# Kernel optimization log

Hardware: AMD Instinct MI355X
Metric: run time of the kernel (lower is better)

The kernel has to match this reference:

```python
import jax, jax.numpy as jnp
import numpy as np

B, SEQ, D = 4, 1024, 1024
H = 16
HD = D // H            # 64, matches cos/sin last dim
S_COLS, TOPK = 8, 2
INTER = 768            # find_multiple(round(1.0 * D * 2 / 3), 256)
EPS = 1e-5


def setup_inputs() -> dict:
    key = jax.random.key(0)
    ks = jax.random.split(key, 6)
    hidden_states = jax.random.normal(ks[0], (B, SEQ, D), jnp.float32)
    # RoPE tables (standard rotary, theta=10000)
    inv_freq = 1.0 / (10000.0 ** (jnp.arange(0, HD, 2, dtype=jnp.float32) / HD))
    freqs = jnp.outer(jnp.arange(SEQ, dtype=jnp.float32), inv_freq)
    emb = jnp.concatenate([freqs, freqs], axis=-1)  # [SEQ, HD]
    cos, sin = jnp.cos(emb), jnp.sin(emb)
    Wr = jax.random.normal(ks[1], (S_COLS, D), jnp.float32) * 0.02
    temperature = jnp.ones((1,), jnp.float32)
    # Stacked per-column TransformerBlock params (bias-free linears)
    Wqkv = jax.random.normal(ks[2], (S_COLS, D, 3 * D), jnp.float32) * 0.02
    Wo = jax.random.normal(ks[3], (S_COLS, D, D), jnp.float32) * 0.02
    Wgu = jax.random.normal(ks[4], (S_COLS, D, 2 * INTER), jnp.float32) * 0.02
    Wd = jax.random.normal(ks[5], (S_COLS, INTER, D), jnp.float32) * 0.02
    return dict(hidden_states=hidden_states, cos=cos, sin=sin, Wr=Wr,
                temperature=temperature, Wqkv=Wqkv, Wo=Wo, Wgu=Wgu, Wd=Wd)


def _rms_norm(x):
    return x * jax.lax.rsqrt(jnp.mean(x * x, axis=-1, keepdims=True) + EPS)


def _rotate_half(x):
    x1, x2 = jnp.split(x, 2, axis=-1)
    return jnp.concatenate([-x2, x1], axis=-1)


def _columns_forward(x, Wqkv, Wo, Wgu, Wd, cos, sin):
    # x: [n, seq, D] dispatched sequences; params gathered per dispatch entry [n, ...]
    n, seq, d = x.shape
    qkv = jnp.einsum('nsd,nde->nse', x, Wqkv)
    q, k, v = jnp.split(qkv, 3, axis=-1)
    q = q.reshape(n, seq, H, HD)
    k = k.reshape(n, seq, H, HD)
    v = v.reshape(n, seq, H, HD)
    c = cos[None, :, None, :]
    s = sin[None, :, None, :]
    q = q * c + _rotate_half(q) * s
    k = k * c + _rotate_half(k) * s
    scores = jnp.einsum('nqhd,nkhd->nhqk', q, k) / jnp.sqrt(jnp.asarray(HD, x.dtype))
    attn = jax.nn.softmax(scores, axis=-1)  # non-causal (HRM-style block)
    ctx = jnp.einsum('nhqk,nkhd->nqhd', attn, v).reshape(n, seq, d)
    attn_out = jnp.einsum('nsd,nde->nse', ctx, Wo)
    x = _rms_norm(x + attn_out)                      # post-norm residual
    gu = jnp.einsum('nsd,nde->nse', x, Wgu)
    gate, up = jnp.split(gu, 2, axis=-1)
    mlp_out = jnp.einsum('nsi,nid->nsd', jax.nn.silu(gate) * up, Wd)
    return _rms_norm(x + mlp_out)


def reference(hidden_states, cos, sin, Wr, temperature, Wqkv, Wo, Wgu, Wd):
    Bn = hidden_states.shape[0]
    temp = jnp.clip(temperature, 0.1, 10.0)
    routing_logits = (hidden_states.mean(axis=1) @ Wr.T) / temp   # [B, S]
    topk_vals, topk_idx = jax.lax.top_k(routing_logits, TOPK)
    weights = jax.nn.softmax(topk_vals, axis=-1)                  # [B, k]
    flat_idx = topk_idx.reshape(-1)                               # [B*k] expert ids
    flat_w = weights.reshape(-1)
    sample_idx = jnp.repeat(jnp.arange(Bn), TOPK)                 # [B*k]
    # Sparse dispatch: exactly B*k block forwards via per-entry param gather
    x_disp = hidden_states[sample_idx]
    col_out = _columns_forward(x_disp, Wqkv[flat_idx], Wo[flat_idx],
                               Wgu[flat_idx], Wd[flat_idx], cos, sin)
    result = jnp.zeros_like(hidden_states).at[sample_idx].add(
        flat_w[:, None, None] * col_out)
    return result, routing_logits
```

## Files before the change

kernel.cpp:

```cpp
#include <hip/hip_runtime.h>
#include <hip/hip_bf16.h>
#include <math.h>

#define B_     4
#define SEQ_   1024
#define D_     1024
#define H_     16
#define NE_    8
#define INTER_ 768
#define EPS_   1e-5f

typedef unsigned short u16;
typedef __attribute__((ext_vector_type(8))) short s8v;
typedef __attribute__((ext_vector_type(4))) short s4v;
typedef __attribute__((ext_vector_type(4))) float f4v;
typedef __attribute__((ext_vector_type(4))) unsigned short u16x4;
typedef __attribute__((ext_vector_type(8))) unsigned short u16x8;

__device__ __forceinline__ u16 f2bf(float x) {
    union { float f; unsigned u; } c; c.f = x;
    unsigned r = (c.u + 0x7FFFu + ((c.u >> 16) & 1u)) >> 16;
    return (u16)r;
}
__device__ __forceinline__ float bf2f(u16 h) {
    union { unsigned u; float f; } c; c.u = ((unsigned)h) << 16;
    return c.f;
}
__device__ __forceinline__ unsigned pk2(float a, float b) {
    union { float f; unsigned u; } x, y; x.f = a; y.f = b;
    return ((x.u + 0x8000u) >> 16) | ((y.u + 0x8000u) & 0xffff0000u);
}

#define GLDS16(gp, lp) \
    __builtin_amdgcn_global_load_lds((const __attribute__((address_space(1))) unsigned int*)(gp), \
                                     (__attribute__((address_space(3))) unsigned int*)(lp), 16, 0, 0)

__global__ void route1(const float* __restrict__ hidden, float* __restrict__ part) {
    int b = blockIdx.x, ch = blockIdx.y, t = threadIdx.x;
    const float* xb = hidden + (size_t)b * SEQ_ * D_ + (size_t)ch * 32 * D_;
    float4 acc = make_float4(0.f, 0.f, 0.f, 0.f);
    for (int r = 0; r < 32; ++r) {
        float4 v = *(const float4*)&xb[(size_t)r * D_ + t * 4];
        acc.x += v.x; acc.y += v.y; acc.z += v.z; acc.w += v.w;
    }
    *(float4*)&part[((size_t)(b * 32 + ch)) * D_ + t * 4] = acc;
}

__global__ void route2(const float* __restrict__ part, const float* __restrict__ Wr,
                       const float* __restrict__ temp, float* __restrict__ out_logits,
                       int* __restrict__ flat_idx, float* __restrict__ flat_w) {
    __shared__ float col[1024];
    __shared__ float sm[8];
    int b = blockIdx.x, t = threadIdx.x;
    float4 s = make_float4(0.f, 0.f, 0.f, 0.f);
    for (int ch = 0; ch < 32; ++ch) {
        float4 v = *(const float4*)&part[((size_t)(b * 32 + ch)) * D_ + t * 4];
        s.x += v.x; s.y += v.y; s.z += v.z; s.w += v.w;
    }
    col[t * 4 + 0] = s.x * (1.f / 1024.f);
    col[t * 4 + 1] = s.y * (1.f / 1024.f);
    col[t * 4 + 2] = s.z * (1.f / 1024.f);
    col[t * 4 + 3] = s.w * (1.f / 1024.f);
    __syncthreads();
    int j = t >> 5, d0 = t & 31;
    float p = 0.f;
    for (int d = d0; d < 1024; d += 32) p += col[d] * Wr[j * 1024 + d];
    for (int off = 16; off >= 1; off >>= 1) p += __shfl_down(p, off, 32);
    if (d0 == 0) sm[j] = p;
    __syncthreads();
    if (t == 0) {
        float tc = temp[0];
        tc = fminf(fmaxf(tc, 0.1f), 10.0f);
        float lg[8];
        for (int jj = 0; jj < 8; ++jj) {
            lg[jj] = sm[jj] / tc;
            out_logits[b * 8 + jj] = lg[jj];
        }
        int i0 = 0; float v0 = lg[0];
        for (int jj = 1; jj < 8; ++jj) if (lg[jj] > v0) { v0 = lg[jj]; i0 = jj; }
        int i1 = -1; float v1 = -1e30f;
        for (int jj = 0; jj < 8; ++jj) if (jj != i0 && lg[jj] > v1) { v1 = lg[jj]; i1 = jj; }
        float e1 = expf(v1 - v0);
        flat_idx[2 * b]     = i0;
        flat_idx[2 * b + 1] = i1;
        flat_w[2 * b]       = 1.0f / (1.0f + e1);
        flat_w[2 * b + 1]   = e1 / (1.0f + e1);
    }
}

__global__ __launch_bounds__(256) void wtrans(const float* __restrict__ W, u16* __restrict__ Wt,
                                              int K, int N) {
    __shared__ float tile[64][65];
    int e = blockIdx.z;
    int k0 = blockIdx.y * 64, n0 = blockIdx.x * 64;
    const float* Wp = W + (size_t)e * K * N;
    u16* Wtp = Wt + (size_t)e * K * N;
    int t = threadIdx.x;
    int kk = t >> 4, ns = t & 15;
#pragma unroll
    for (int p = 0; p < 4; ++p) {
        float4 v = *(const float4*)&Wp[(size_t)(k0 + kk + p * 16) * N + n0 + ns * 4];
        tile[kk + p * 16][ns * 4 + 0] = v.x;
        tile[kk + p * 16][ns * 4 + 1] = v.y;
        tile[kk + p * 16][ns * 4 + 2] = v.z;
        tile[kk + p * 16][ns * 4 + 3] = v.w;
    }
    __syncthreads();
    int nn = t >> 3, ks = t & 7;
#pragma unroll
    for (int p = 0; p < 2; ++p) {
        u16x8 o;
#pragma unroll
        for (int jj = 0; jj < 8; ++jj) o[jj] = f2bf(tile[ks * 8 + jj][nn + p * 32]);
        *(u16x8*)&Wtp[(size_t)(n0 + nn + p * 32) * K + k0 + ks * 8] = o;
    }
}

__global__ void cast_hidden(const float* __restrict__ x, u16* __restrict__ xb) {
    size_t i = (size_t)blockIdx.x * 256 + threadIdx.x;
    float4 v = *(const float4*)&x[i * 4];
    u16x4 o = {f2bf(v.x), f2bf(v.y), f2bf(v.z), f2bf(v.w)};
    *(u16x4*)&xb[i * 4] = o;
}

#define GEMM_CORE(A, Wt, K)                                                                 \
    f4v acc[4][4];                                                                          \
    _Pragma("unroll") for (int i = 0; i < 4; ++i)                                           \
        _Pragma("unroll") for (int jj = 0; jj < 4; ++jj) acc[i][jj] = (f4v){0.f,0.f,0.f,0.f}; \
    for (int k0 = 0; k0 < K; k0 += 32) {                                                    \
        _Pragma("unroll") for (int it = 0; it < 2; ++it) {                                  \
            int p = it * 256 + w * 64 + lane;                                               \
            int row = p >> 2, seg = (p & 3) ^ ((row >> 1) & 3);                             \
            GLDS16(A  + (size_t)(m0 + row) * K + k0 + seg * 8, As + (size_t)(it*256 + w*64) * 8); \
            GLDS16(Wt + (size_t)(n0 + row) * K + k0 + seg * 8, Bs + (size_t)(it*256 + w*64) * 8); \
        }                                                                                   \
        __syncthreads();                                                                    \
        s8v af[4], bfr[4];                                                                  \
        _Pragma("unroll") for (int ti = 0; ti < 4; ++ti) {                                  \
            int r = wm + ti * 16 + c;                                                       \
            af[ti]  = *(const s8v*)&As[r * 32 + (g ^ ((r >> 1) & 3)) * 8];                   \
        }                                                                                   \
        _Pragma("unroll") for (int tj = 0; tj < 4; ++tj) {                                  \
            int r = wn + tj * 16 + c;                                                       \
            bfr[tj] = *(const s8v*)&Bs[r * 32 + (g ^ ((r >> 1) & 3)) * 8];                   \
        }                                                                                   \
        _Pragma("unroll") for (int ti = 0; ti < 4; ++ti)                                    \
            _Pragma("unroll") for (int tj = 0; tj < 4; ++tj)                                \
                acc[ti][tj] = __builtin_amdgcn_mfma_f32_16x16x32_bf16(af[ti], bfr[tj], acc[ti][tj], 0, 0, 0); \
        __syncthreads();                                                                    \
    }

template<int OUTBF>
__global__ __launch_bounds__(256) void gemm_bf16(const u16* __restrict__ Abase,
                                                 const u16* __restrict__ Wtbase,
                                                 void* __restrict__ Cb,
                                                 const int* __restrict__ flat_idx,
                                                 int M, int N, int K, int aDiv) {
    __shared__ __align__(16) u16 As[128 * 32];
    __shared__ __align__(16) u16 Bs[128 * 32];
    int e = blockIdx.z;
    const u16* A  = Abase + (size_t)(e / aDiv) * M * K;
    const u16* Wt = Wtbase + (size_t)flat_idx[e] * N * K;
    int m0 = blockIdx.y * 128, n0 = blockIdx.x * 128;
    int t = threadIdx.x, lane = t & 63, w = t >> 6;
    int g = lane >> 4, c = lane & 15;
    int wm = (w >> 1) * 64, wn = (w & 1) * 64;

    GEMM_CORE(A, Wt, K)

    if (OUTBF) {
        u16* C = (u16*)Cb + (size_t)e * M * N;
#pragma unroll
        for (int ti = 0; ti < 4; ++ti)
#pragma unroll
            for (int tj = 0; tj < 4; ++tj)
#pragma unroll
                for (int i = 0; i < 4; ++i)
                    C[(size_t)(m0 + wm + ti * 16 + g * 4 + i) * N + n0 + wn + tj * 16 + c] = f2bf(acc[ti][tj][i]);
    } else {
        float* C = (float*)Cb + (size_t)e * M * N;
#pragma unroll
        for (int ti = 0; ti < 4; ++ti)
#pragma unroll
            for (int tj = 0; tj < 4; ++tj)
#pragma unroll
                for (int i = 0; i < 4; ++i)
                    C[(size_t)(m0 + wm + ti * 16 + g * 4 + i) * N + n0 + wn + tj * 16 + c] = acc[ti][tj][i];
    }
}

__global__ __launch_bounds__(256) void gemm_qkv(const u16* __restrict__ Abase,
                                                const u16* __restrict__ Wtbase,
                                                const int* __restrict__ flat_idx,
                                                const float* __restrict__ cosb,
                                                const float* __restrict__ sinb,
                                                u16* __restrict__ Qb, u16* __restrict__ Kb,
                                                u16* __restrict__ Vb) {
    __shared__ __align__(16) u16 As[128 * 32];
    __shared__ __align__(16) u16 Bs[128 * 32];
    const int K = 1024, N = 3072;
    int e = blockIdx.z;
    const u16* A  = Abase + (size_t)(e >> 1) * 1024 * K;
    const u16* Wt = Wtbase + (size_t)flat_idx[e] * N * K;
    int m0 = blockIdx.y * 128, n0 = blockIdx.x * 128;
    int t = threadIdx.x, lane = t & 63, w = t >> 6;
    int g = lane >> 4, c = lane & 15;
    int wm = (w >> 1) * 64, wn = (w & 1) * 64;

    GEMM_CORE(A, Wt, K)

    int col0 = n0 + wn;
    int sb = m0 + wm + g * 4;
    if (col0 < 2048) {
        bool isq = col0 < 1024;
        u16* dst = isq ? Qb : Kb;
        int h = (col0 & 1023) >> 6;
        const float scl = isq ? 0.125f * 1.44269504f : 1.0f;
#pragma unroll
        for (int ti = 0; ti < 4; ++ti)
#pragma unroll
            for (int i = 0; i < 4; ++i) {
                int s = sb + ti * 16 + i;
                size_t ob = ((size_t)(e * 1024) + s) * 1024 + h * 64;
#pragma unroll
                for (int tj = 0; tj < 2; ++tj) {
                    int d = tj * 16 + c;
                    float x1 = acc[ti][tj][i], x2 = acc[ti][tj + 2][i];
                    float c1 = cosb[s * 64 + d],      s1 = sinb[s * 64 + d];
                    float c2 = cosb[s * 64 + d + 32], s2 = sinb[s * 64 + d + 32];
                    dst[ob + d]      = f2bf((x1 * c1 - x2 * s1) * scl);
                    dst[ob + d + 32] = f2bf((x2 * c2 + x1 * s2) * scl);
                }
            }
    } else {
        int vcol = col0 - 2048;
#pragma unroll
        for (int ti = 0; ti < 4; ++ti)
#pragma unroll
            for (int tj = 0; tj < 4; ++tj)
#pragma unroll
                for (int i = 0; i < 4; ++i)
                    Vb[((size_t)(e * 1024) + sb + ti * 16 + i) * 1024 + vcol + tj * 16 + c] = f2bf(acc[ti][tj][i]);
    }
}

__global__ __launch_bounds__(256) void vtrans(const u16* __restrict__ Vb, u16* __restrict__ Vtg) {
    __shared__ __align__(16) u16 tile[64 * 72];
    int s0 = blockIdx.x * 64;
    int eh = blockIdx.y;
    int e = eh >> 4, h = eh & 15;
    int t = threadIdx.x;
#pragma unroll
    for (int it = 0; it < 2; ++it) {
        int p = it * 256 + t;
        int sr = p >> 3, ds = p & 7;
        u16x8 v = *(const u16x8*)&Vb[((size_t)(e * 1024) + s0 + sr) * 1024 + h * 64 + ds * 8];
        *(u16x8*)&tile[sr * 72 + ds * 8] = v;
    }
    __syncthreads();
#pragma unroll
    for (int it = 0; it < 2; ++it) {
        int p = it * 256 + t;
        int d = p >> 3, ks = p & 7;
        u16x8 o;
#pragma unroll
        for (int jj = 0; jj < 8; ++jj) o[jj] = tile[(ks * 8 + jj) * 72 + d];
        *(u16x8*)&Vtg[((size_t)((e * 16 + h) * 64) + d) * 1024 + s0 + ks * 8] = o;
    }
}

__global__ __launch_bounds__(256) void attn_mfma(const u16* __restrict__ Qb, const u16* __restrict__ Kb,
                                                 const u16* __restrict__ Vtg, u16* __restrict__ ctx) {
    __shared__ __align__(16) u16 Ks[64 * 64];
    __shared__ __align__(16) u16 Vt[64 * 64];
    int e = blockIdx.x, h = blockIdx.y, qt = blockIdx.z;
    int t = threadIdx.x, lane = t & 63, w = t >> 6;
    int g = lane >> 4, c = lane & 15;
    int q0 = qt * 64 + w * 16;

    s8v qf[2];
#pragma unroll
    for (int ks = 0; ks < 2; ++ks)
        qf[ks] = *(const s8v*)&Qb[((size_t)(e * 1024) + q0 + c) * 1024 + h * 64 + ks * 32 + g * 8];

    f4v O[4];
#pragma unroll
    for (int tj = 0; tj < 4; ++tj) O[tj] = (f4v){0.f, 0.f, 0.f, 0.f};
    f4v liacc = (f4v){0.f, 0.f, 0.f, 0.f};
    const s4v vone = {(short)0x3F80, (short)0x3F80, (short)0x3F80, (short)0x3F80};

    for (int kt = 0; kt < 16; ++kt) {
#pragma unroll
        for (int it = 0; it < 2; ++it) {
            int p = it * 256 + w * 64 + lane;
            int row = p >> 3, ss = p & 7;
            GLDS16(Kb + ((size_t)(e * 1024 + kt * 64 + row)) * 1024 + h * 64 + (ss ^ (row & 7)) * 8,
                   Ks + (size_t)(it * 256 + w * 64) * 8);
            GLDS16(Vtg + ((size_t)((e * 16 + h) * 64 + row)) * 1024 + kt * 64 + (ss ^ (row & 7)) * 8,
                   Vt + (size_t)(it * 256 + w * 64) * 8);
        }
        __syncthreads();

        f4v st[4];
#pragma unroll
        for (int tj = 0; tj < 4; ++tj) st[tj] = (f4v){0.f, 0.f, 0.f, 0.f};
#pragma unroll
        for (int ks = 0; ks < 2; ++ks)
#pragma unroll
            for (int tj = 0; tj < 4; ++tj) {
                int kvl = tj * 16 + c;
                s8v kf = *(const s8v*)&Ks[kvl * 64 + (((ks * 4 + g) ^ (kvl & 7)) * 8)];
                st[tj] = __builtin_amdgcn_mfma_f32_16x16x32_bf16(kf, qf[ks], st[tj], 0, 0, 0);
            }

        s4v pf[4];
#pragma unroll
        for (int tj = 0; tj < 4; ++tj) {
            float p0 = __builtin_amdgcn_exp2f(st[tj][0]);
            float p1 = __builtin_amdgcn_exp2f(st[tj][1]);
            float p2 = __builtin_amdgcn_exp2f(st[tj][2]);
            float p3 = __builtin_amdgcn_exp2f(st[tj][3]);
            union { unsigned u[2]; s4v v; } pu;
            pu.u[0] = pk2(p0, p1);
            pu.u[1] = pk2(p2, p3);
            pf[tj] = pu.v;
        }

#pragma unroll
        for (int tjC = 0; tjC < 4; ++tjC) {
            liacc = __builtin_amdgcn_mfma_f32_16x16x16bf16_1k(pf[tjC], vone, liacc, 0, 0, 0);
#pragma unroll
            for (int tjd = 0; tjd < 4; ++tjd) {
                int d = tjd * 16 + c;
                int sd = tjC * 2 + (g >> 1);
                s4v vf = *(const s4v*)&Vt[d * 64 + ((sd ^ (d & 7)) * 8) + (g & 1) * 4];
                O[tjd] = __builtin_amdgcn_mfma_f32_16x16x16bf16_1k(pf[tjC], vf, O[tjd], 0, 0, 0);
            }
        }
        __syncthreads();
    }
#pragma unroll
    for (int i = 0; i < 4; ++i) {
        float linv = 1.0f / liacc[i];
        size_t rbase = ((size_t)(e * 1024) + q0 + g * 4 + i) * 1024 + h * 64;
#pragma unroll
        for (int tjd = 0; tjd < 4; ++tjd)
            ctx[rbase + tjd * 16 + c] = f2bf(O[tjd][i] * linv);
    }
}

__global__ void add_rmsnorm(const float* __restrict__ hidden, const float* __restrict__ ao,
                            u16* __restrict__ xnb) {
    int row = blockIdx.x;
    int e = row >> 10;
    int b = e >> 1;
    int s = row & 1023;
    const float* xr = hidden + (((size_t)b * SEQ_ + s) << 10);
    const float* ar = ao + ((size_t)row << 10);
    u16* o = xnb + ((size_t)row << 10);
    int t = threadIdx.x;
    float v[4];
    float ss = 0.f;
#pragma unroll
    for (int i = 0; i < 4; ++i) {
        v[i] = xr[t + i * 256] + ar[t + i * 256];
        ss += v[i] * v[i];
    }
    for (int off = 32; off >= 1; off >>= 1) ss += __shfl_down(ss, off, 64);
    __shared__ float wred[4];
    if ((t & 63) == 0) wred[t >> 6] = ss;
    __syncthreads();
    float tot = wred[0] + wred[1] + wred[2] + wred[3];
    float scale = rsqrtf(tot * (1.0f / 1024.0f) + EPS_);
#pragma unroll
    for (int i = 0; i < 4; ++i) o[t + i * 256] = f2bf(v[i] * scale);
}

__global__ void silu_mul(const u16* __restrict__ gub, u16* __restrict__ act) {
    int idx = blockIdx.x * 256 + threadIdx.x;
    int col8 = idx % 96;
    int row  = idx / 96;
    u16x8 gv = *(const u16x8*)&gub[(size_t)row * 1536 + col8 * 8];
    u16x8 uv = *(const u16x8*)&gub[(size_t)row * 1536 + 768 + col8 * 8];
    u16x8 o;
#pragma unroll
    for (int jj = 0; jj < 8; ++jj) {
        float gt = bf2f(gv[jj]), u = bf2f(uv[jj]);
        o[jj] = f2bf(gt / (1.f + __expf(-gt)) * u);
    }
    *(u16x8*)&act[(size_t)row * 768 + col8 * 8] = o;
}

__global__ void final_kernel(const u16* __restrict__ xnb, const float* __restrict__ mlp,
                             const float* __restrict__ flat_w, float* __restrict__ out) {
    int row = blockIdx.x;
    int b = row >> 10;
    int s = row & 1023;
    int t = threadIdx.x;
    __shared__ float wred[4];
    float res[4] = {0.f, 0.f, 0.f, 0.f};
    for (int j = 0; j < 2; ++j) {
        int e = 2 * b + j;
        size_t off = (((size_t)e * SEQ_ + s) << 10);
        const u16* xr = xnb + off;
        const float* mr = mlp + off;
        float v[4];
        float ss = 0.f;
#pragma unroll
        for (int i = 0; i < 4; ++i) {
            v[i] = bf2f(xr[t + i * 256]) + mr[t + i * 256];
            ss += v[i] * v[i];
        }
        for (int off2 = 32; off2 >= 1; off2 >>= 1) ss += __shfl_down(ss, off2, 64);
        if ((t & 63) == 0) wred[t >> 6] = ss;
        __syncthreads();
        float tot = wred[0] + wred[1] + wred[2] + wred[3];
        float scale = rsqrtf(tot * (1.0f / 1024.0f) + EPS_);
        float wgt = flat_w[e];
#pragma unroll
        for (int i = 0; i < 4; ++i) res[i] += wgt * v[i] * scale;
        __syncthreads();
    }
    float* o = out + ((size_t)row << 10);
#pragma unroll
    for (int i = 0; i < 4; ++i) o[t + i * 256] = res[i];
}

extern "C" void kernel_launch(void* const* d_in, const int* in_sizes, int n_in,
                              void* d_out, int out_size, void* d_ws, size_t ws_size,
                              hipStream_t stream) {
    const float* hidden = (const float*)d_in[0];
    const float* cosb   = (const float*)d_in[1];
    const float* sinb   = (const float*)d_in[2];
    const float* Wr     = (const float*)d_in[3];
    const float* temp   = (const float*)d_in[4];
    const float* Wqkv   = (const float*)d_in[5];
    const float* Wo     = (const float*)d_in[6];
    const float* Wgu    = (const float*)d_in[7];
    const float* Wd     = (const float*)d_in[8];
    float* out = (float*)d_out;
    float* out_logits = out + (size_t)B_ * SEQ_ * D_;

    char* base = (char*)d_ws;
    int*   flat_idx = (int*)base;
    float* flat_w   = (float*)(base + 128);
    float* routeP   = (float*)(base + 4096);
    size_t off = (size_t)1 << 20;
    u16* WqkvT = (u16*)(base + off); off += (size_t)8 * 3072 * 1024 * 2;
    u16* WoT   = (u16*)(base + off); off += (size_t)8 * 1024 * 1024 * 2;
    u16* WguT  = (u16*)(base + off); off += (size_t)8 * 1536 * 1024 * 2;
    u16* WdT   = (u16*)(base + off); off += (size_t)8 * 1024 * 768 * 2;
    u16* hb    = (u16*)(base + off); off += (size_t)4 * 1024 * 1024 * 2;
    u16* scr   = (u16*)(base + off); off += (size_t)8 * 1024 * 3072 * 2;
    u16* Qb    = (u16*)(base + off); off += (size_t)8 * 1024 * 1024 * 2;
    u16* Kb    = (u16*)(base + off); off += (size_t)8 * 1024 * 1024 * 2;
    u16* Vtg   = (u16*)(base + off); off += (size_t)8 * 1024 * 1024 * 2;
    u16* ctxb  = (u16*)(base + off); off += (size_t)8 * 1024 * 1024 * 2;
    float* R1  = (float*)(base + off); off += (size_t)8 * 1024 * 1024 * 4;
    u16* xnb   = (u16*)(base + off); off += (size_t)8 * 1024 * 1024 * 2;
    u16* gub   = scr;
    u16* actb  = scr + (size_t)8 * 1024 * 1536;
    u16* Vb    = (u16*)R1;

    route1<<<dim3(4, 32), 256, 0, stream>>>(hidden, routeP);
    route2<<<4, 256, 0, stream>>>(routeP, Wr, temp, out_logits, flat_idx, flat_w);
    cast_hidden<<<4096, 256, 0, stream>>>(hidden, hb);
    wtrans<<<dim3(48, 16, 8), 256, 0, stream>>>(Wqkv, WqkvT, 1024, 3072);
    wtrans<<<dim3(16, 16, 8), 256, 0, stream>>>(Wo, WoT, 1024, 1024);
    wtrans<<<dim3(24, 16, 8), 256, 0, stream>>>(Wgu, WguT, 1024, 1536);
    wtrans<<<dim3(16, 12, 8), 256, 0, stream>>>(Wd, WdT, 768, 1024);

    gemm_qkv<<<dim3(24, 8, 8), 256, 0, stream>>>(hb, WqkvT, flat_idx, cosb, sinb, Qb, Kb, Vb);
    vtrans<<<dim3(16, 128), 256, 0, stream>>>(Vb, Vtg);
    attn_mfma<<<dim3(8, 16, 16), 256, 0, stream>>>(Qb, Kb, Vtg, ctxb);
    gemm_bf16<0><<<dim3(8, 8, 8), 256, 0, stream>>>(ctxb, WoT, R1, flat_idx, 1024, 1024, 1024, 1);
    add_rmsnorm<<<NE_ * SEQ_, 256, 0, stream>>>(hidden, R1, xnb);
    gemm_bf16<1><<<dim3(12, 8, 8), 256, 0, stream>>>(xnb, WguT, gub, flat_idx, 1024, 1536, 1024, 1);
    silu_mul<<<3072, 256, 0, stream>>>(gub, actb);
    gemm_bf16<0><<<dim3(8, 8, 8), 256, 0, stream>>>(actb, WdT, R1, flat_idx, 1024, 1024, 768, 1);
    final_kernel<<<B_ * SEQ_, 256, 0, stream>>>(xnb, R1, flat_w, out);
}
```

Measured before the change: 573.2 us.

## Fuse SiLU into gate/up GEMM, merge weight transposes, bf16 intermediates

Several unrelated changes. The hidden-state cast moves into the routing reduction kernel, and the four weight-transpose launches merge into one kernel. That kernel interleaves the gate/up columns in 16-wide groups so the gate/up GEMM epilogue can apply SiLU*up directly, which removes the separate silu_mul pass and its intermediate buffer. The GEMM outputs for the attention projection and down projection become bf16 instead of fp32, and the norm kernels use vectorized loads. This reduces memory traffic and launch count, at the cost of extra bf16 rounding on the residual paths.

```diff
diff --git a/kernel.cpp b/kernel.cpp
--- a/kernel.cpp
+++ b/kernel.cpp
@@ -35,13 +35,17 @@
     __builtin_amdgcn_global_load_lds((const __attribute__((address_space(1))) unsigned int*)(gp), \
                                      (__attribute__((address_space(3))) unsigned int*)(lp), 16, 0, 0)
 
-__global__ void route1(const float* __restrict__ hidden, float* __restrict__ part) {
+__global__ void route1(const float* __restrict__ hidden, float* __restrict__ part,
+                       u16* __restrict__ hb) {
     int b = blockIdx.x, ch = blockIdx.y, t = threadIdx.x;
     const float* xb = hidden + (size_t)b * SEQ_ * D_ + (size_t)ch * 32 * D_;
+    u16* ho = hb + (size_t)b * SEQ_ * D_ + (size_t)ch * 32 * D_;
     float4 acc = make_float4(0.f, 0.f, 0.f, 0.f);
     for (int r = 0; r < 32; ++r) {
         float4 v = *(const float4*)&xb[(size_t)r * D_ + t * 4];
         acc.x += v.x; acc.y += v.y; acc.z += v.z; acc.w += v.w;
+        u16x4 o = {f2bf(v.x), f2bf(v.y), f2bf(v.z), f2bf(v.w)};
+        *(u16x4*)&ho[(size_t)r * D_ + t * 4] = o;
     }
     *(float4*)&part[((size_t)(b * 32 + ch)) * D_ + t * 4] = acc;
 }
@@ -88,11 +92,25 @@
     }
 }
 
-__global__ __launch_bounds__(256) void wtrans(const float* __restrict__ W, u16* __restrict__ Wt,
-                                              int K, int N) {
+__global__ __launch_bounds__(256) void wtrans_all(const float* __restrict__ Wqkv,
+                                                  const float* __restrict__ Wo,
+                                                  const float* __restrict__ Wgu,
+                                                  const float* __restrict__ Wd,
+                                                  u16* __restrict__ WqkvT, u16* __restrict__ WoT,
+                                                  u16* __restrict__ WguT, u16* __restrict__ WdT) {
+    int bid = blockIdx.x;
+    const float* W; u16* Wt; int K, N, nx, gu = 0;
+    if (bid < 6144)      { W = Wqkv; Wt = WqkvT; K = 1024; N = 3072; nx = 48; }
+    else if (bid < 8192) { bid -= 6144;  W = Wo;  Wt = WoT;  K = 1024; N = 1024; nx = 16; }
+    else if (bid < 11264){ bid -= 8192;  W = Wgu; Wt = WguT; K = 1024; N = 1536; nx = 24; gu = 1; }
+    else                 { bid -= 11264; W = Wd;  Wt = WdT;  K = 768;  N = 1024; nx = 16; }
+    int x = bid % nx; bid /= nx;
+    int ny = K >> 6;
+    int y = bid % ny;
+    int e = bid / ny;
+
     __shared__ float tile[64][65];
-    int e = blockIdx.z;
-    int k0 = blockIdx.y * 64, n0 = blockIdx.x * 64;
+    int k0 = y * 64, n0 = x * 64;
     const float* Wp = W + (size_t)e * K * N;
     u16* Wtp = Wt + (size_t)e * K * N;
     int t = threadIdx.x;
@@ -109,18 +127,15 @@
     int nn = t >> 3, ks = t & 7;
 #pragma unroll
     for (int p = 0; p < 2; ++p) {
+        int n = n0 + nn + p * 32;
+        int nd = n;
+        if (gu) nd = (n < 768) ? ((n >> 4) << 5) + (n & 15)
+                               : (((n - 768) >> 4) << 5) + 16 + (n & 15);
         u16x8 o;
 #pragma unroll
         for (int jj = 0; jj < 8; ++jj) o[jj] = f2bf(tile[ks * 8 + jj][nn + p * 32]);
-        *(u16x8*)&Wtp[(size_t)(n0 + nn + p * 32) * K + k0 + ks * 8] = o;
-    }
-}
-
-__global__ void cast_hidden(const float* __restrict__ x, u16* __restrict__ xb) {
-    size_t i = (size_t)blockIdx.x * 256 + threadIdx.x;
-    float4 v = *(const float4*)&x[i * 4];
-    u16x4 o = {f2bf(v.x), f2bf(v.y), f2bf(v.z), f2bf(v.w)};
-    *(u16x4*)&xb[i * 4] = o;
+        *(u16x8*)&Wtp[(size_t)nd * K + k0 + ks * 8] = o;
+    }
 }
 
 #define GEMM_CORE(A, Wt, K)                                                                 \
@@ -150,10 +165,9 @@
         __syncthreads();                                                                    \
     }
 
-template<int OUTBF>
 __global__ __launch_bounds__(256) void gemm_bf16(const u16* __restrict__ Abase,
                                                  const u16* __restrict__ Wtbase,
-                                                 void* __restrict__ Cb,
+                                                 u16* __restrict__ Cb,
                                                  const int* __restrict__ flat_idx,
                                                  int M, int N, int K, int aDiv) {
     __shared__ __align__(16) u16 As[128 * 32];
@@ -168,25 +182,14 @@
 
     GEMM_CORE(A, Wt, K)
 
-    if (OUTBF) {
-        u16* C = (u16*)Cb + (size_t)e * M * N;
-#pragma unroll
-        for (int ti = 0; ti < 4; ++ti)
-#pragma unroll
-            for (int tj = 0; tj < 4; ++tj)
-#pragma unroll
-                for (int i = 0; i < 4; ++i)
-                    C[(size_t)(m0 + wm + ti * 16 + g * 4 + i) * N + n0 + wn + tj * 16 + c] = f2bf(acc[ti][tj][i]);
-    } else {
-        float* C = (float*)Cb + (size_t)e * M * N;
-#pragma unroll
-        for (int ti = 0; ti < 4; ++ti)
-#pragma unroll
-            for (int tj = 0; tj < 4; ++tj)
-#pragma unroll
-                for (int i = 0; i < 4; ++i)
-                    C[(size_t)(m0 + wm + ti * 16 + g * 4 + i) * N + n0 + wn + tj * 16 + c] = acc[ti][tj][i];
-    }
+    u16* C = Cb + (size_t)e * M * N;
+#pragma unroll
+    for (int ti = 0; ti < 4; ++ti)
+#pragma unroll
+        for (int tj = 0; tj < 4; ++tj)
+#pragma unroll
+            for (int i = 0; i < 4; ++i)
+                C[(size_t)(m0 + wm + ti * 16 + g * 4 + i) * N + n0 + wn + tj * 16 + c] = f2bf(acc[ti][tj][i]);
 }
 
 __global__ __launch_bounds__(256) void gemm_qkv(const u16* __restrict__ Abase,
@@ -244,6 +247,40 @@
     }
 }
 
+__global__ __launch_bounds__(256) void gemm_wgu_silu(const u16* __restrict__ Abase,
+                                                     const u16* __restrict__ Wtbase,
+                                                     u16* __restrict__ act,
+                                                     const int* __restrict__ flat_idx) {
+    __shared__ __align__(16) u16 As[128 * 32];
+    __shared__ __align__(16) u16 Bs[128 * 32];
+    const int K = 1024, N = 1536;
+    int e = blockIdx.z;
+    const u16* A  = Abase + (size_t)e * 1024 * K;
+    const u16* Wt = Wtbase + (size_t)flat_idx[e] * N * K;
+    int m0 = blockIdx.y * 128, n0 = blockIdx.x * 128;
+    int t = threadIdx.x, lane = t & 63, w = t >> 6;
+    int g = lane >> 4, c = lane & 15;
+    int wm = (w >> 1) * 64, wn = (w & 1) * 64;
+
+    GEMM_CORE(A, Wt, K)
+
+    int col0 = n0 + wn;
+    int oc0 = (col0 >> 1) + c;
+    int sb = m0 + wm + g * 4;
+#pragma unroll
+    for (int ti = 0; ti < 4; ++ti)
+#pragma unroll
+        for (int i = 0; i < 4; ++i) {
+            size_t rb = ((size_t)(e * 1024) + sb + ti * 16 + i) * 768;
+#pragma unroll
+            for (int pr = 0; pr < 2; ++pr) {
+                float gt = acc[ti][pr * 2][i];
+                float up = acc[ti][pr * 2 + 1][i];
+                act[rb + oc0 + pr * 16] = f2bf(gt / (1.f + __expf(-gt)) * up);
+            }
+        }
+}
+
 __global__ __launch_bounds__(256) void vtrans(const u16* __restrict__ Vb, u16* __restrict__ Vtg) {
     __shared__ __align__(16) u16 tile[64 * 72];
     int s0 = blockIdx.x * 64;
@@ -349,21 +386,23 @@
     }
 }
 
-__global__ void add_rmsnorm(const float* __restrict__ hidden, const float* __restrict__ ao,
+__global__ void add_rmsnorm(const u16* __restrict__ hb, const u16* __restrict__ aob,
                             u16* __restrict__ xnb) {
     int row = blockIdx.x;
     int e = row >> 10;
     int b = e >> 1;
     int s = row & 1023;
-    const float* xr = hidden + (((size_t)b * SEQ_ + s) << 10);
-    const float* ar = ao + ((size_t)row << 10);
+    const u16* xr = hb + (((size_t)b * SEQ_ + s) << 10);
+    const u16* ar = aob + ((size_t)row << 10);
     u16* o = xnb + ((size_t)row << 10);
     int t = threadIdx.x;
+    u16x4 xv = *(const u16x4*)&xr[t * 4];
+    u16x4 av = *(const u16x4*)&ar[t * 4];
     float v[4];
     float ss = 0.f;
 #pragma unroll
     for (int i = 0; i < 4; ++i) {
-        v[i] = xr[t + i * 256] + ar[t + i * 256];
+        v[i] = bf2f(xv[i]) + bf2f(av[i]);
         ss += v[i] * v[i];
     }
     for (int off = 32; off >= 1; off >>= 1) ss += __shfl_down(ss, off, 64);
@@ -372,26 +411,13 @@
     __syncthreads();
     float tot = wred[0] + wred[1] + wred[2] + wred[3];
     float scale = rsqrtf(tot * (1.0f / 1024.0f) + EPS_);
-#pragma unroll
-    for (int i = 0; i < 4; ++i) o[t + i * 256] = f2bf(v[i] * scale);
-}
-
-__global__ void silu_mul(const u16* __restrict__ gub, u16* __restrict__ act) {
-    int idx = blockIdx.x * 256 + threadIdx.x;
-    int col8 = idx % 96;
-    int row  = idx / 96;
-    u16x8 gv = *(const u16x8*)&gub[(size_t)row * 1536 + col8 * 8];
-    u16x8 uv = *(const u16x8*)&gub[(size_t)row * 1536 + 768 + col8 * 8];
-    u16x8 o;
-#pragma unroll
-    for (int jj = 0; jj < 8; ++jj) {
-        float gt = bf2f(gv[jj]), u = bf2f(uv[jj]);
-        o[jj] = f2bf(gt / (1.f + __expf(-gt)) * u);
-    }
-    *(u16x8*)&act[(size_t)row * 768 + col8 * 8] = o;
-}
-
-__global__ void final_kernel(const u16* __restrict__ xnb, const float* __restrict__ mlp,
+    u16x4 ov;
+#pragma unroll
+    for (int i = 0; i < 4; ++i) ov[i] = f2bf(v[i] * scale);
+    *(u16x4*)&o[t * 4] = ov;
+}
+
+__global__ void final_kernel(const u16* __restrict__ xnb, const u16* __restrict__ mlpb,
                              const float* __restrict__ flat_w, float* __restrict__ out) {
     int row = blockIdx.x;
     int b = row >> 10;
@@ -402,13 +428,13 @@
     for (int j = 0; j < 2; ++j) {
         int e = 2 * b + j;
         size_t off = (((size_t)e * SEQ_ + s) << 10);
-        const u16* xr = xnb + off;
-        const float* mr = mlp + off;
+        u16x4 xv = *(const u16x4*)&xnb[off + t * 4];
+        u16x4 mv = *(const u16x4*)&mlpb[off + t * 4];
         float v[4];
         float ss = 0.f;
 #pragma unroll
         for (int i = 0; i < 4; ++i) {
-            v[i] = bf2f(xr[t + i * 256]) + mr[t + i * 256];
+            v[i] = bf2f(xv[i]) + bf2f(mv[i]);
             ss += v[i] * v[i];
         }
         for (int off2 = 32; off2 >= 1; off2 >>= 1) ss += __shfl_down(ss, off2, 64);
@@ -422,8 +448,7 @@
         __syncthreads();
     }
     float* o = out + ((size_t)row << 10);
-#pragma unroll
-    for (int i = 0; i < 4; ++i) o[t + i * 256] = res[i];
+    *(float4*)&o[t * 4] = make_float4(res[0], res[1], res[2], res[3]);
 }
 
 extern "C" void kernel_launch(void* const* d_in, const int* in_sizes, int n_in,
@@ -451,32 +476,26 @@
     u16* WguT  = (u16*)(base + off); off += (size_t)8 * 1536 * 1024 * 2;
     u16* WdT   = (u16*)(base + off); off += (size_t)8 * 1024 * 768 * 2;
     u16* hb    = (u16*)(base + off); off += (size_t)4 * 1024 * 1024 * 2;
-    u16* scr   = (u16*)(base + off); off += (size_t)8 * 1024 * 3072 * 2;
     u16* Qb    = (u16*)(base + off); off += (size_t)8 * 1024 * 1024 * 2;
     u16* Kb    = (u16*)(base + off); off += (size_t)8 * 1024 * 1024 * 2;
+    u16* Vb    = (u16*)(base + off); off += (size_t)8 * 1024 * 1024 * 2;
     u16* Vtg   = (u16*)(base + off); off += (size_t)8 * 1024 * 1024 * 2;
     u16* ctxb  = (u16*)(base + off); off += (size_t)8 * 1024 * 1024 * 2;
-    float* R1  = (float*)(base + off); off += (size_t)8 * 1024 * 1024 * 4;
+    u16* aob   = (u16*)(base + off); off += (size_t)8 * 1024 * 1024 * 2;
     u16* xnb   = (u16*)(base + off); off += (size_t)8 * 1024 * 1024 * 2;
-    u16* gub   = scr;
-    u16* actb  = scr + (size_t)8 * 1024 * 1536;
-    u16* Vb    = (u16*)R1;
-
-    route1<<<dim3(4, 32), 256, 0, stream>>>(hidden, routeP);
+    u16* actb  = (u16*)(base + off); off += (size_t)8 * 1024 * 768 * 2;
+    u16* mlpb  = (u16*)(base + off); off += (size_t)8 * 1024 * 1024 * 2;
+
+    route1<<<dim3(4, 32), 256, 0, stream>>>(hidden, routeP, hb);
     route2<<<4, 256, 0, stream>>>(routeP, Wr, temp, out_logits, flat_idx, flat_w);
-    cast_hidden<<<4096, 256, 0, stream>>>(hidden, hb);
-    wtrans<<<dim3(48, 16, 8), 256, 0, stream>>>(Wqkv, WqkvT, 1024, 3072);
-    wtrans<<<dim3(16, 16, 8), 256, 0, stream>>>(Wo, WoT, 1024, 1024);
-    wtrans<<<dim3(24, 16, 8), 256, 0, stream>>>(Wgu, WguT, 1024, 1536);
-    wtrans<<<dim3(16, 12, 8), 256, 0, stream>>>(Wd, WdT, 768, 1024);
+    wtrans_all<<<12800, 256, 0, stream>>>(Wqkv, Wo, Wgu, Wd, WqkvT, WoT, WguT, WdT);
 
     gemm_qkv<<<dim3(24, 8, 8), 256, 0, stream>>>(hb, WqkvT, flat_idx, cosb, sinb, Qb, Kb, Vb);
     vtrans<<<dim3(16, 128), 256, 0, stream>>>(Vb, Vtg);
     attn_mfma<<<dim3(8, 16, 16), 256, 0, stream>>>(Qb, Kb, Vtg, ctxb);
-    gemm_bf16<0><<<dim3(8, 8, 8), 256, 0, stream>>>(ctxb, WoT, R1, flat_idx, 1024, 1024, 1024, 1);
-    add_rmsnorm<<<NE_ * SEQ_, 256, 0, stream>>>(hidden, R1, xnb);
-    gemm_bf16<1><<<dim3(12, 8, 8), 256, 0, stream>>>(xnb, WguT, gub, flat_idx, 1024, 1536, 1024, 1);
-    silu_mul<<<3072, 256, 0, stream>>>(gub, actb);
-    gemm_bf16<0><<<dim3(8, 8, 8), 256, 0, stream>>>(actb, WdT, R1, flat_idx, 1024, 1024, 768, 1);
-    final_kernel<<<B_ * SEQ_, 256, 0, stream>>>(xnb, R1, flat_w, out);
-}
+    gemm_bf16<<<dim3(8, 8, 8), 256, 0, stream>>>(ctxb, WoT, aob, flat_idx, 1024, 1024, 1024, 1);
+    add_rmsnorm<<<NE_ * SEQ_, 256, 0, stream>>>(hb, aob, xnb);
+    gemm_wgu_silu<<<dim3(12, 8, 8), 256, 0, stream>>>(xnb, WguT, actb, flat_idx);
+    gemm_bf16<<<dim3(8, 8, 8), 256, 0, stream>>>(actb, WdT, mlpb, flat_idx, 1024, 1024, 768, 1);
+    final_kernel<<<B_ * SEQ_, 256, 0, stream>>>(xnb, mlpb, flat_w, out);
+}
```

New measurement: 546.8 us. -4.6%, faster.
